# Performance work log

Hardware: AMD Instinct MI355X
Metric: run time of the kernel (lower is better)

The kernel has to match this reference:

```python
import jax, jax.numpy as jnp
import numpy as np
import math

B, R, D = 1, 2, 256
NH, NL, NP, ZA = 8, 1, 8, 4
H = W = 128
Q = H * W
HD = D // NH


def _bilinear(v, loc, Hl, Wl):
    # v: [BH, Hl*Wl, hd]; loc: [BH, Q, P, 2] normalized to [0,1]
    x = loc[..., 0] * Wl - 0.5
    y = loc[..., 1] * Hl - 0.5
    x0f = jnp.floor(x); y0f = jnp.floor(y)
    wx = (x - x0f)[..., None]; wy = (y - y0f)[..., None]
    x0 = x0f.astype(jnp.int32); y0 = y0f.astype(jnp.int32)
    def corner(iy, ix):
        valid = (iy >= 0) & (iy < Hl) & (ix >= 0) & (ix < Wl)
        idx = jnp.clip(iy, 0, Hl - 1) * Wl + jnp.clip(ix, 0, Wl - 1)
        g = jax.vmap(lambda vb, ib: vb[ib])(v, idx)  # [BH,Q,P,hd]
        return g * valid[..., None].astype(v.dtype)
    g00 = corner(y0, x0); g01 = corner(y0, x0 + 1)
    g10 = corner(y0 + 1, x0); g11 = corner(y0 + 1, x0 + 1)
    return (g00 * (1 - wx) + g01 * wx) * (1 - wy) + (g10 * (1 - wx) + g11 * wx) * wy


def setup_inputs() -> dict:
    key = jax.random.key(0)
    ks = jax.random.split(key, 12)
    query = jax.random.normal(ks[0], (B, Q, D), jnp.float32)
    value = jax.random.normal(ks[1], (B * R, Q, D), jnp.float32)
    reference_points = jax.random.uniform(ks[2], (R, Q, ZA, 2), jnp.float32)
    spatial_shapes = jnp.array([[H, W]], jnp.int32)
    # sampling_offsets: zero-ish weight + directional grid bias (as in init_weights)
    W_off = 0.01 * jax.random.normal(ks[3], (NH * NL * NP * 2, D), jnp.float32)
    thetas = jnp.arange(NH, dtype=jnp.float32) * (2.0 * math.pi / NH)
    grid = jnp.stack([jnp.cos(thetas), jnp.sin(thetas)], -1)
    grid = grid / jnp.max(jnp.abs(grid), axis=-1, keepdims=True)
    grid = jnp.tile(grid[:, None, None, :], (1, NL, NP, 1))
    grid = grid * (jnp.arange(1, NP + 1, dtype=jnp.float32)[None, None, :, None])
    b_off = grid.reshape(-1)
    W_attn = 0.01 * jax.random.normal(ks[4], (NH * NL * NP, D), jnp.float32)
    b_attn = 0.01 * jax.random.normal(ks[5], (NH * NL * NP,), jnp.float32)
    s = 1.0 / np.sqrt(D)
    W_val = s * jax.random.normal(ks[6], (D, D), jnp.float32)
    b_val = jnp.zeros((D,), jnp.float32)
    W_out = s * jax.random.normal(ks[7], (D, D), jnp.float32)
    b_out = jnp.zeros((D,), jnp.float32)
    return {"query": query, "value": value, "reference_points": reference_points,
            "spatial_shapes": spatial_shapes, "W_off": W_off, "b_off": b_off,
            "W_attn": W_attn, "b_attn": b_attn, "W_val": W_val, "b_val": b_val,
            "W_out": W_out, "b_out": b_out}


def reference(query, value, reference_points, spatial_shapes,
              W_off, b_off, W_attn, b_attn, W_val, b_val, W_out, b_out):
    shapes = np.asarray(spatial_shapes)  # static level shapes
    residual = query
    Bq, nq, d = query.shape
    Rr, _, za, _ = reference_points.shape
    # rebatch query/reference_points over histories -> batch Bq*Rr (== value batch)
    q = jnp.broadcast_to(query[:, None], (Bq, Rr, nq, d)).reshape(Bq * Rr, nq, d)
    rp = jnp.broadcast_to(reference_points[None], (Bq, Rr, nq, za, 2)).reshape(Bq * Rr, nq, za, 2)
    bs = value.shape[0]
    v = (value @ W_val.T + b_val).reshape(bs, -1, NH, HD)
    off = (q @ W_off.T + b_off).reshape(bs, nq, NH, NL, NP, 2)
    aw = jax.nn.softmax((q @ W_attn.T + b_attn).reshape(bs, nq, NH, NL * NP), axis=-1)
    aw = aw.reshape(bs, nq, NH, NL, NP)
    norm = jnp.stack([shapes[:, 1].astype(np.float32), shapes[:, 0].astype(np.float32)], -1)  # [NL,2] = (W,H)
    off = off / norm[None, None, None, :, None, :]
    off = off.reshape(bs, nq, NH, NL, NP // za, za, 2)
    loc = rp[:, :, None, None, None, :, :] + off  # [bs,nq,NH,NL,NP//za,za,2]
    loc = loc.reshape(bs, nq, NH, NL, NP, 2)
    # multi-scale deformable attention (gather + bilinear + weighted sum)
    starts = np.concatenate([[0], np.cumsum(shapes[:, 0] * shapes[:, 1])])
    out = jnp.zeros((bs * NH, nq, HD), v.dtype)
    for l in range(NL):
        Hl, Wl = int(shapes[l, 0]), int(shapes[l, 1])
        vl = v[:, starts[l]:starts[l + 1]].transpose(0, 2, 1, 3).reshape(bs * NH, Hl * Wl, HD)
        locl = loc[:, :, :, l].transpose(0, 2, 1, 3, 4).reshape(bs * NH, nq, NP, 2)
        sampled = _bilinear(vl, locl, Hl, Wl)  # [bs*NH, nq, NP, hd]
        awl = aw[:, :, :, l].transpose(0, 2, 1, 3).reshape(bs * NH, nq, NP)
        out = out + jnp.einsum('bqph,bqp->bqh', sampled, awl)
    out = out.reshape(bs, NH, nq, HD).transpose(0, 2, 1, 3).reshape(bs, nq, d)
    out = out.mean(0, keepdims=True)  # mean over history-batch dim -> [1,nq,d]
    out = out @ W_out.T + b_out
    return out + residual  # dropout is identity in eval
```

## Files before the change

kernel.cpp:

```cpp
#include <hip/hip_runtime.h>
#include <hip/hip_bf16.h>
#include <hip/hip_fp16.h>

#define QN 16384
#define DK 256

typedef float f4_t __attribute__((ext_vector_type(4)));
typedef short s16x8 __attribute__((ext_vector_type(8)));
typedef short s16x4 __attribute__((ext_vector_type(4)));
typedef unsigned int u32;
typedef u32 u32x4 __attribute__((ext_vector_type(4)));
typedef __fp16 h2_t __attribute__((ext_vector_type(2)));

__device__ inline short f2bf(float f){
  __hip_bfloat16 h = __float2bfloat16(f);
  return __builtin_bit_cast(short, h);
}
__device__ inline short f2h16(float f){
  __half h = __float2half(f);
  return __builtin_bit_cast(short, h);
}
__device__ inline float dot2h(u32 a, u32 b, float c){
#if __has_builtin(__builtin_amdgcn_fdot2)
  return __builtin_amdgcn_fdot2(__builtin_bit_cast(h2_t, a),
                                __builtin_bit_cast(h2_t, b), c, false);
#else
  h2_t ha = __builtin_bit_cast(h2_t, a), hb = __builtin_bit_cast(h2_t, b);
  return c + (float)ha[0] * (float)hb[0] + (float)ha[1] * (float)hb[1];
#endif
}
__device__ inline u32 pk2h(float a, float b){
#if __has_builtin(__builtin_amdgcn_cvt_pkrtz)
  h2_t r = __builtin_amdgcn_cvt_pkrtz(a, b);
  return __builtin_bit_cast(u32, r);
#else
  return (u32)__builtin_bit_cast(unsigned short, __float2half(a)) |
         ((u32)__builtin_bit_cast(unsigned short, __float2half(b)) << 16);
#endif
}
__device__ inline u32 bperm(u32 s0, u32 s1, u32 sel){
  return __builtin_amdgcn_perm(s0, s1, sel);
}

__global__ __launch_bounds__(256) void k_convw(const float* __restrict__ Wv,
    const float* __restrict__ Woff, const float* __restrict__ Wattn,
    const float* __restrict__ Wout, short* __restrict__ Wbf){
  const int row = blockIdx.x;
  const int c = threadIdx.x;
  const float* src;
  if (row < 256)       src = Wv    + (size_t)row * DK;
  else if (row < 384)  src = Woff  + (size_t)(row - 256) * DK;
  else if (row < 448)  src = Wattn + (size_t)(row - 384) * DK;
  else                 src = Wout  + (size_t)(row - 448) * DK;
  Wbf[(size_t)row * DK + c] = f2bf(src[c]);
}

__global__ __launch_bounds__(256, 2) void k_gemm_val(const float* __restrict__ A,
    const short* __restrict__ Bw, const float* __restrict__ bval,
    short* __restrict__ vhf){
  __shared__ short As[64 * 256];
  __shared__ short Bs[64 * 256];
  const int tid = threadIdx.x;
  const int lane = tid & 63, wv = tid >> 6;
  const int r16 = lane & 15, kh = lane >> 4;
  const int swsel = (r16 & 7) << 4;
  const int mbase = blockIdx.x * 64;

  #pragma unroll
  for (int i = 0; i < 16; ++i){
    const int lin = i * 256 + tid;
    const int r = lin >> 6, ck = lin & 63;
    const f4_t v = *(const f4_t*)(A + (size_t)(mbase + r) * DK + ck * 4);
    s16x4 o = { f2bf(v[0]), f2bf(v[1]), f2bf(v[2]), f2bf(v[3]) };
    *(s16x4*)((char*)As + r * 512 + ((ck * 8) ^ ((r & 7) << 4))) = o;
  }
  s16x8 breg[8];
  #pragma unroll
  for (int i = 0; i < 8; ++i){
    const int lin = i * 256 + tid;
    const int n = lin >> 5, ck = lin & 31;
    breg[i] = *(const s16x8*)(Bw + (size_t)n * DK + ck * 8);
  }
  __syncthreads();

  for (int cg = 0; cg < 4; ++cg){
    #pragma unroll
    for (int i = 0; i < 8; ++i){
      const int lin = i * 256 + tid;
      const int n = lin >> 5, ck = lin & 31;
      *(s16x8*)((char*)Bs + n * 512 + ((ck * 16) ^ ((n & 7) << 4))) = breg[i];
    }
    __syncthreads();
    if (cg < 3){
      #pragma unroll
      for (int i = 0; i < 8; ++i){
        const int lin = i * 256 + tid;
        const int n = lin >> 5, ck = lin & 31;
        breg[i] = *(const s16x8*)(Bw + (size_t)((cg + 1) * 64 + n) * DK + ck * 8);
      }
    }
    f4_t acc[4];
    #pragma unroll
    for (int i = 0; i < 4; ++i) acc[i] = (f4_t){0.f, 0.f, 0.f, 0.f};
    #pragma unroll
    for (int kk = 0; kk < 8; ++kk){
      const int kb = kh * 16 + kk * 64;
      const s16x8 a = *(const s16x8*)((char*)As + (wv * 16 + r16) * 512 + (kb ^ swsel));
      #pragma unroll
      for (int nt = 0; nt < 4; ++nt){
        const s16x8 b = *(const s16x8*)((char*)Bs + (nt * 16 + r16) * 512 + (kb ^ swsel));
        acc[nt] = __builtin_amdgcn_mfma_f32_16x16x32_bf16(a, b, acc[nt], 0, 0, 0);
      }
    }
    #pragma unroll
    for (int nt = 0; nt < 4; ++nt){
      const int n = cg * 64 + nt * 16 + r16;
      const int h = n >> 5, hd = n & 31;
      const float bv = bval[n];
      #pragma unroll
      for (int rix = 0; rix < 4; ++rix){
        const int m = mbase + wv * 16 + kh * 4 + rix;
        const int r = m >> 14, pix = m & (QN - 1);
        vhf[(size_t)((r * 8 + h) * QN + pix) * 32 + hd] = f2h16(acc[nt][rix] + bv);
      }
    }
    __syncthreads();
  }
}

__global__ __launch_bounds__(256, 2) void k_gemm_oa(const float* __restrict__ A,
    const short* __restrict__ Bw, const float* __restrict__ boff,
    const float* __restrict__ battn, float* __restrict__ offw,
    float* __restrict__ logit){
  __shared__ short As[32 * 256];
  __shared__ short Bs[64 * 256];
  const int tid = threadIdx.x;
  const int lane = tid & 63, wv = tid >> 6;
  const int r16 = lane & 15, kh = lane >> 4;
  const int mg = wv & 1, ch = wv >> 1;
  const int swsel = (r16 & 7) << 4;
  const int mbase = blockIdx.x * 32;

  #pragma unroll
  for (int i = 0; i < 8; ++i){
    const int lin = i * 256 + tid;
    const int r = lin >> 6, ck = lin & 63;
    const f4_t v = *(const f4_t*)(A + (size_t)(mbase + r) * DK + ck * 4);
    s16x4 o = { f2bf(v[0]), f2bf(v[1]), f2bf(v[2]), f2bf(v[3]) };
    *(s16x4*)((char*)As + r * 512 + ((ck * 8) ^ ((r & 7) << 4))) = o;
  }
  s16x8 breg[8];
  #pragma unroll
  for (int i = 0; i < 8; ++i){
    const int lin = i * 256 + tid;
    const int n = lin >> 5, ck = lin & 31;
    breg[i] = *(const s16x8*)(Bw + (size_t)n * DK + ck * 8);
  }
  __syncthreads();

  for (int cg = 0; cg < 3; ++cg){
    #pragma unroll
    for (int i = 0; i < 8; ++i){
      const int lin = i * 256 + tid;
      const int n = lin >> 5, ck = lin & 31;
      *(s16x8*)((char*)Bs + n * 512 + ((ck * 16) ^ ((n & 7) << 4))) = breg[i];
    }
    __syncthreads();
    if (cg < 2){
      #pragma unroll
      for (int i = 0; i < 8; ++i){
        const int lin = i * 256 + tid;
        const int n = lin >> 5, ck = lin & 31;
        breg[i] = *(const s16x8*)(Bw + (size_t)((cg + 1) * 64 + n) * DK + ck * 8);
      }
    }
    f4_t acc[2];
    acc[0] = (f4_t){0.f,0.f,0.f,0.f}; acc[1] = (f4_t){0.f,0.f,0.f,0.f};
    #pragma unroll
    for (int kk = 0; kk < 8; ++kk){
      const int kb = kh * 16 + kk * 64;
      const s16x8 a = *(const s16x8*)((char*)As + (mg * 16 + r16) * 512 + (kb ^ swsel));
      #pragma unroll
      for (int nt = 0; nt < 2; ++nt){
        const s16x8 b = *(const s16x8*)((char*)Bs + (ch * 32 + nt * 16 + r16) * 512 + (kb ^ swsel));
        acc[nt] = __builtin_amdgcn_mfma_f32_16x16x32_bf16(a, b, acc[nt], 0, 0, 0);
      }
    }
    #pragma unroll
    for (int nt = 0; nt < 2; ++nt){
      const int n = cg * 64 + ch * 32 + nt * 16 + r16;
      #pragma unroll
      for (int rix = 0; rix < 4; ++rix){
        const int m = mbase + mg * 16 + kh * 4 + rix;
        const float v = acc[nt][rix];
        if (n < 128) offw[(size_t)m * 128 + n] = v + boff[n];
        else         logit[(size_t)m * 64 + (n - 128)] = v + battn[n - 128];
      }
    }
    __syncthreads();
  }
}

__global__ __launch_bounds__(256, 2) void k_gemm_out(const short* __restrict__ Ab,
    const short* __restrict__ Bw, const float* __restrict__ bout,
    const float* __restrict__ query, float* __restrict__ out){
  __shared__ short As[32 * 256];
  __shared__ short Bs[64 * 256];
  const int tid = threadIdx.x;
  const int lane = tid & 63, wv = tid >> 6;
  const int r16 = lane & 15, kh = lane >> 4;
  const int mg = wv & 1, ch = wv >> 1;
  const int swsel = (r16 & 7) << 4;
  const int mbase = blockIdx.x * 32;

  #pragma unroll
  for (int i = 0; i < 4; ++i){
    const int lin = i * 256 + tid;
    const int r = lin >> 5, ck = lin & 31;
    const s16x8 v = *(const s16x8*)(Ab + (size_t)(mbase + r) * DK + ck * 8);
    *(s16x8*)((char*)As + r * 512 + ((ck * 16) ^ ((r & 7) << 4))) = v;
  }
  s16x8 breg[8];
  #pragma unroll
  for (int i = 0; i < 8; ++i){
    const int lin = i * 256 + tid;
    const int n = lin >> 5, ck = lin & 31;
    breg[i] = *(const s16x8*)(Bw + (size_t)n * DK + ck * 8);
  }
  __syncthreads();

  for (int cg = 0; cg < 4; ++cg){
    #pragma unroll
    for (int i = 0; i < 8; ++i){
      const int lin = i * 256 + tid;
      const int n = lin >> 5, ck = lin & 31;
      *(s16x8*)((char*)Bs + n * 512 + ((ck * 16) ^ ((n & 7) << 4))) = breg[i];
    }
    __syncthreads();
    if (cg < 3){
      #pragma unroll
      for (int i = 0; i < 8; ++i){
        const int lin = i * 256 + tid;
        const int n = lin >> 5, ck = lin & 31;
        breg[i] = *(const s16x8*)(Bw + (size_t)((cg + 1) * 64 + n) * DK + ck * 8);
      }
    }
    f4_t acc[2];
    acc[0] = (f4_t){0.f,0.f,0.f,0.f}; acc[1] = (f4_t){0.f,0.f,0.f,0.f};
    #pragma unroll
    for (int kk = 0; kk < 8; ++kk){
      const int kb = kh * 16 + kk * 64;
      const s16x8 a = *(const s16x8*)((char*)As + (mg * 16 + r16) * 512 + (kb ^ swsel));
      #pragma unroll
      for (int nt = 0; nt < 2; ++nt){
        const s16x8 b = *(const s16x8*)((char*)Bs + (ch * 32 + nt * 16 + r16) * 512 + (kb ^ swsel));
        acc[nt] = __builtin_amdgcn_mfma_f32_16x16x32_bf16(a, b, acc[nt], 0, 0, 0);
      }
    }
    #pragma unroll
    for (int nt = 0; nt < 2; ++nt){
      const int n = cg * 64 + ch * 32 + nt * 16 + r16;
      const float bo = bout[n];
      #pragma unroll
      for (int rix = 0; rix < 4; ++rix){
        const int m = mbase + mg * 16 + kh * 4 + rix;
        out[(size_t)m * DK + n] = acc[nt][rix] + bo + query[(size_t)m * DK + n];
      }
    }
    __syncthreads();
  }
}

__device__ inline void mkw(float rx, float ry, float ox, float oy, float awp,
                           u32& word, u32& pk01, u32& pk23){
  const float x = fmaf(rx, 128.f, ox) - 0.5f;
  const float y = fmaf(ry, 128.f, oy) - 0.5f;
  const float xf = floorf(x), yf = floorf(y);
  const float wx = x - xf, wy = y - yf;
  const int ix = (int)xf, iy = (int)yf;
  float xw0 = 1.f - wx, xw1 = wx, yw0 = 1.f - wy, yw1 = wy;
  if (ix < 0 || ix > 127)   xw0 = 0.f;
  if (ix < -1 || ix > 126)  xw1 = 0.f;
  if (iy < 0 || iy > 127)   yw0 = 0.f;
  if (iy < -1 || iy > 126)  yw1 = 0.f;
  const int ix0 = min(max(ix, 0), 127), ix1 = min(max(ix + 1, 0), 127);
  const int iy0 = min(max(iy, 0), 127), iy1 = min(max(iy + 1, 0), 127);
  const float t0 = awp * yw0, t1 = awp * yw1;
  pk01 = pk2h(t0 * xw0, t0 * xw1);
  pk23 = pk2h(t1 * xw0, t1 * xw1);
  word = (u32)(iy0 * 128 + ix0) | ((u32)(ix1 - ix0) << 16) | ((u32)(iy1 - iy0) << 17);
}

__global__ __launch_bounds__(256) void k_sampler(const float* __restrict__ rp,
    const float* __restrict__ offw, const float* __restrict__ logit,
    const short* __restrict__ vhf, short* __restrict__ O2b){
  const int tid = threadIdx.x;
  const int j3 = tid & 7;
  const int cj = j3 & 3;
  const int px = j3 >> 2;
  const int grp = tid >> 3;
  const int lane = tid & 63;
  const int glane8 = lane & ~7;
  const int h = blockIdx.x & 7;
  const int q = (blockIdx.x >> 3) * 32 + grp;
  const u32 cjof = (u32)cj * 8;
  const u32 selw = px ? 0x03020706u : 0x01000504u;

  const float* lp = logit + (size_t)q * 64 + h * 8;
  const float l = lp[j3];
  float m = l;
  m = fmaxf(m, __shfl_xor(m, 1)); m = fmaxf(m, __shfl_xor(m, 2)); m = fmaxf(m, __shfl_xor(m, 4));
  const float e = __expf(l - m);
  float ssum = e;
  ssum += __shfl_xor(ssum, 1); ssum += __shfl_xor(ssum, 2); ssum += __shfl_xor(ssum, 4);
  const float awp = e * (0.5f / ssum);

  const float* offp = offw + (size_t)q * 128 + h * 16;
  const float ox = offp[2 * j3], oy = offp[2 * j3 + 1];
  const int za2 = (j3 & 3) * 2;
  const float rx0 = rp[(size_t)q * 8 + za2],        ry0 = rp[(size_t)q * 8 + za2 + 1];
  const float rx1 = rp[(size_t)(QN + q) * 8 + za2], ry1 = rp[(size_t)(QN + q) * 8 + za2 + 1];

  u32 wrdA, pkA01, pkA23, wrdB, pkB01, pkB23;
  mkw(rx0, ry0, ox, oy, awp, wrdA, pkA01, pkA23);
  mkw(rx1, ry1, ox, oy, awp, wrdB, pkB01, pkB23);

  const short* vb0 = vhf + (size_t)(h * QN) * 32;
  const short* vb1 = vhf + (size_t)((8 + h) * QN) * 32;

  float acc[8] = {0.f,0.f,0.f,0.f,0.f,0.f,0.f,0.f};

#define STEP(S, WRD, PK01, PK23, VB) do{                                    \
    const int srcl_ = glane8 | ((S) & 7);                                   \
    const u32 wd_  = __shfl((WRD),  srcl_);                                 \
    const u32 w01_ = __shfl((PK01), srcl_);                                 \
    const u32 w23_ = __shfl((PK23), srcl_);                                 \
    const u32 wp_  = bperm(w01_, w23_, selw);     \
    const u32 o0_  = (wd_ & 0xFFFFu) * 32u + cjof                           \
                   + (px ? ((wd_ >> 11) & 32u) : 0u);                       \
    const u32 o1_  = o0_ + ((wd_ >> 17) & 1u) * 4096u;                      \
    const u32x4 cA_ = *(const u32x4*)((VB) + o0_);              \
    const u32x4 cB_ = *(const u32x4*)((VB) + o1_);              \
    _Pragma("unroll")                                                       \
    for (int e_ = 0; e_ < 4; ++e_){                                         \
      const u32 pl_ = bperm(cA_[e_], cB_[e_], 0x01000504u);                 \
      const u32 ph_ = bperm(cA_[e_], cB_[e_], 0x03020706u);                 \
      acc[2*e_]   = dot2h(pl_, wp_, acc[2*e_]);                             \
      acc[2*e_+1] = dot2h(ph_, wp_, acc[2*e_+1]);                           \
    }                                                                       \
  }while(0)

  STEP(0,  wrdA, pkA01, pkA23, vb0); STEP(1,  wrdA, pkA01, pkA23, vb0);
  STEP(2,  wrdA, pkA01, pkA23, vb0); STEP(3,  wrdA, pkA01, pkA23, vb0);
  STEP(4,  wrdA, pkA01, pkA23, vb0); STEP(5,  wrdA, pkA01, pkA23, vb0);
  STEP(6,  wrdA, pkA01, pkA23, vb0); STEP(7,  wrdA, pkA01, pkA23, vb0);
  STEP(8,  wrdB, pkB01, pkB23, vb1); STEP(9,  wrdB, pkB01, pkB23, vb1);
  STEP(10, wrdB, pkB01, pkB23, vb1); STEP(11, wrdB, pkB01, pkB23, vb1);
  STEP(12, wrdB, pkB01, pkB23, vb1); STEP(13, wrdB, pkB01, pkB23, vb1);
  STEP(14, wrdB, pkB01, pkB23, vb1); STEP(15, wrdB, pkB01, pkB23, vb1);
#undef STEP

  #pragma unroll
  for (int i = 0; i < 8; ++i) acc[i] += __shfl_xor(acc[i], 4);
  if (px == 0){
    s16x8 o = { f2bf(acc[0]), f2bf(acc[1]), f2bf(acc[2]), f2bf(acc[3]),
                f2bf(acc[4]), f2bf(acc[5]), f2bf(acc[6]), f2bf(acc[7]) };
    *(s16x8*)(O2b + (size_t)q * DK + h * 32 + cj * 8) = o;
  }
}

extern "C" void kernel_launch(void* const* d_in, const int* in_sizes, int n_in,
                              void* d_out, int out_size, void* d_ws, size_t ws_size,
                              hipStream_t stream) {
  const float* query = (const float*)d_in[0];
  const float* value = (const float*)d_in[1];
  const float* refpt = (const float*)d_in[2];
  const float* W_off  = (const float*)d_in[4];
  const float* b_off  = (const float*)d_in[5];
  const float* W_attn = (const float*)d_in[6];
  const float* b_attn = (const float*)d_in[7];
  const float* W_val  = (const float*)d_in[8];
  const float* b_val  = (const float*)d_in[9];
  const float* W_out  = (const float*)d_in[10];
  const float* b_out  = (const float*)d_in[11];
  float* out = (float*)d_out;

  char* ws = (char*)d_ws;
  short* Wbf  = (short*)(ws);
  short* vhf  = (short*)(ws + 360448);
  float* offw = (float*)(ws + 17137664);
  float* logit= (float*)(ws + 25526272);
  short* O2b  = (short*)(ws + 29720576);

  k_convw   <<<dim3(704),  dim3(256), 0, stream>>>(W_val, W_off, W_attn, W_out, Wbf);
  k_gemm_val<<<dim3(512),  dim3(256), 0, stream>>>(value, Wbf, b_val, vhf);
  k_gemm_oa <<<dim3(512),  dim3(256), 0, stream>>>(query, Wbf + 256 * DK, b_off, b_attn, offw, logit);
  k_sampler <<<dim3(4096), dim3(256), 0, stream>>>(refpt, offw, logit, vhf, O2b);
  k_gemm_out<<<dim3(512),  dim3(256), 0, stream>>>(O2b, Wbf + 448 * DK, b_out, query, out);
}
```

Measured before the change: 75.63 us.

## Merge value and offset/attention projections into one launch, pipeline sampler gathers

Combines the value projection GEMM and the offset/attention-logit GEMM into a single kernel that branches on block index, removing one launch and letting both projections run concurrently across the GPU. The weight-conversion kernel now processes 16 elements per thread with vectorized loads, using far fewer blocks. In the sampler, the gather loads for each sampling step are issued a few steps ahead of their use (software pipelining) to hide memory latency. The pipelining raises register pressure, and the merged kernel mixes two block shapes whose shared-memory and register footprints may differ.

```diff
diff --git a/kernel.cpp b/kernel.cpp
--- a/kernel.cpp
+++ b/kernel.cpp
@@ -45,159 +45,161 @@
 __global__ __launch_bounds__(256) void k_convw(const float* __restrict__ Wv,
     const float* __restrict__ Woff, const float* __restrict__ Wattn,
     const float* __restrict__ Wout, short* __restrict__ Wbf){
-  const int row = blockIdx.x;
-  const int c = threadIdx.x;
-  const float* src;
-  if (row < 256)       src = Wv    + (size_t)row * DK;
-  else if (row < 384)  src = Woff  + (size_t)(row - 256) * DK;
-  else if (row < 448)  src = Wattn + (size_t)(row - 384) * DK;
-  else                 src = Wout  + (size_t)(row - 448) * DK;
-  Wbf[(size_t)row * DK + c] = f2bf(src[c]);
-}
-
-__global__ __launch_bounds__(256, 2) void k_gemm_val(const float* __restrict__ A,
-    const short* __restrict__ Bw, const float* __restrict__ bval,
-    short* __restrict__ vhf){
+  const int base = (blockIdx.x * 256 + threadIdx.x) * 16;
+  #pragma unroll
+  for (int c = 0; c < 4; ++c){
+    const int e = base + c * 4;
+    const int row = e >> 8, col = e & 255;
+    const float* src;
+    int r = row;
+    if (row < 256)       src = Wv    + (size_t)r * DK;
+    else if (row < 384){ src = Woff  + (size_t)(r - 256) * DK; }
+    else if (row < 448){ src = Wattn + (size_t)(r - 384) * DK; }
+    else               { src = Wout  + (size_t)(r - 448) * DK; }
+    const f4_t v = *(const f4_t*)(src + col);
+    s16x4 o = { f2bf(v[0]), f2bf(v[1]), f2bf(v[2]), f2bf(v[3]) };
+    *(s16x4*)(Wbf + e) = o;
+  }
+}
+
+__global__ __launch_bounds__(256, 2) void k_proj(const float* __restrict__ value,
+    const float* __restrict__ query, const short* __restrict__ Wbf,
+    const float* __restrict__ bval, const float* __restrict__ boff,
+    const float* __restrict__ battn, short* __restrict__ vhf,
+    float* __restrict__ offw, float* __restrict__ logit){
   __shared__ short As[64 * 256];
   __shared__ short Bs[64 * 256];
   const int tid = threadIdx.x;
   const int lane = tid & 63, wv = tid >> 6;
   const int r16 = lane & 15, kh = lane >> 4;
   const int swsel = (r16 & 7) << 4;
-  const int mbase = blockIdx.x * 64;
-
-  #pragma unroll
-  for (int i = 0; i < 16; ++i){
-    const int lin = i * 256 + tid;
-    const int r = lin >> 6, ck = lin & 63;
-    const f4_t v = *(const f4_t*)(A + (size_t)(mbase + r) * DK + ck * 4);
-    s16x4 o = { f2bf(v[0]), f2bf(v[1]), f2bf(v[2]), f2bf(v[3]) };
-    *(s16x4*)((char*)As + r * 512 + ((ck * 8) ^ ((r & 7) << 4))) = o;
-  }
-  s16x8 breg[8];
-  #pragma unroll
-  for (int i = 0; i < 8; ++i){
-    const int lin = i * 256 + tid;
-    const int n = lin >> 5, ck = lin & 31;
-    breg[i] = *(const s16x8*)(Bw + (size_t)n * DK + ck * 8);
-  }
-  __syncthreads();
-
-  for (int cg = 0; cg < 4; ++cg){
+  const int bid = blockIdx.x;
+
+  if (bid < 512){
+    const float* A = value;
+    const short* Bw = Wbf;
+    const int mbase = bid * 64;
+    #pragma unroll
+    for (int i = 0; i < 16; ++i){
+      const int lin = i * 256 + tid;
+      const int r = lin >> 6, ck = lin & 63;
+      const f4_t v = *(const f4_t*)(A + (size_t)(mbase + r) * DK + ck * 4);
+      s16x4 o = { f2bf(v[0]), f2bf(v[1]), f2bf(v[2]), f2bf(v[3]) };
+      *(s16x4*)((char*)As + r * 512 + ((ck * 8) ^ ((r & 7) << 4))) = o;
+    }
+    s16x8 breg[8];
     #pragma unroll
     for (int i = 0; i < 8; ++i){
       const int lin = i * 256 + tid;
       const int n = lin >> 5, ck = lin & 31;
-      *(s16x8*)((char*)Bs + n * 512 + ((ck * 16) ^ ((n & 7) << 4))) = breg[i];
+      breg[i] = *(const s16x8*)(Bw + (size_t)n * DK + ck * 8);
     }
     __syncthreads();
-    if (cg < 3){
+    for (int cg = 0; cg < 4; ++cg){
       #pragma unroll
       for (int i = 0; i < 8; ++i){
         const int lin = i * 256 + tid;
         const int n = lin >> 5, ck = lin & 31;
-        breg[i] = *(const s16x8*)(Bw + (size_t)((cg + 1) * 64 + n) * DK + ck * 8);
-      }
-    }
-    f4_t acc[4];
-    #pragma unroll
-    for (int i = 0; i < 4; ++i) acc[i] = (f4_t){0.f, 0.f, 0.f, 0.f};
-    #pragma unroll
-    for (int kk = 0; kk < 8; ++kk){
-      const int kb = kh * 16 + kk * 64;
-      const s16x8 a = *(const s16x8*)((char*)As + (wv * 16 + r16) * 512 + (kb ^ swsel));
+        *(s16x8*)((char*)Bs + n * 512 + ((ck * 16) ^ ((n & 7) << 4))) = breg[i];
+      }
+      __syncthreads();
+      if (cg < 3){
+        #pragma unroll
+        for (int i = 0; i < 8; ++i){
+          const int lin = i * 256 + tid;
+          const int n = lin >> 5, ck = lin & 31;
+          breg[i] = *(const s16x8*)(Bw + (size_t)((cg + 1) * 64 + n) * DK + ck * 8);
+        }
+      }
+      f4_t acc[4];
+      #pragma unroll
+      for (int i = 0; i < 4; ++i) acc[i] = (f4_t){0.f, 0.f, 0.f, 0.f};
+      #pragma unroll
+      for (int kk = 0; kk < 8; ++kk){
+        const int kb = kh * 16 + kk * 64;
+        const s16x8 a = *(const s16x8*)((char*)As + (wv * 16 + r16) * 512 + (kb ^ swsel));
+        #pragma unroll
+        for (int nt = 0; nt < 4; ++nt){
+          const s16x8 b = *(const s16x8*)((char*)Bs + (nt * 16 + r16) * 512 + (kb ^ swsel));
+          acc[nt] = __builtin_amdgcn_mfma_f32_16x16x32_bf16(a, b, acc[nt], 0, 0, 0);
+        }
+      }
       #pragma unroll
       for (int nt = 0; nt < 4; ++nt){
-        const s16x8 b = *(const s16x8*)((char*)Bs + (nt * 16 + r16) * 512 + (kb ^ swsel));
-        acc[nt] = __builtin_amdgcn_mfma_f32_16x16x32_bf16(a, b, acc[nt], 0, 0, 0);
-      }
-    }
-    #pragma unroll
-    for (int nt = 0; nt < 4; ++nt){
-      const int n = cg * 64 + nt * 16 + r16;
-      const int h = n >> 5, hd = n & 31;
-      const float bv = bval[n];
-      #pragma unroll
-      for (int rix = 0; rix < 4; ++rix){
-        const int m = mbase + wv * 16 + kh * 4 + rix;
-        const int r = m >> 14, pix = m & (QN - 1);
-        vhf[(size_t)((r * 8 + h) * QN + pix) * 32 + hd] = f2h16(acc[nt][rix] + bv);
-      }
-    }
-    __syncthreads();
-  }
-}
-
-__global__ __launch_bounds__(256, 2) void k_gemm_oa(const float* __restrict__ A,
-    const short* __restrict__ Bw, const float* __restrict__ boff,
-    const float* __restrict__ battn, float* __restrict__ offw,
-    float* __restrict__ logit){
-  __shared__ short As[32 * 256];
-  __shared__ short Bs[64 * 256];
-  const int tid = threadIdx.x;
-  const int lane = tid & 63, wv = tid >> 6;
-  const int r16 = lane & 15, kh = lane >> 4;
-  const int mg = wv & 1, ch = wv >> 1;
-  const int swsel = (r16 & 7) << 4;
-  const int mbase = blockIdx.x * 32;
-
-  #pragma unroll
-  for (int i = 0; i < 8; ++i){
-    const int lin = i * 256 + tid;
-    const int r = lin >> 6, ck = lin & 63;
-    const f4_t v = *(const f4_t*)(A + (size_t)(mbase + r) * DK + ck * 4);
-    s16x4 o = { f2bf(v[0]), f2bf(v[1]), f2bf(v[2]), f2bf(v[3]) };
-    *(s16x4*)((char*)As + r * 512 + ((ck * 8) ^ ((r & 7) << 4))) = o;
-  }
-  s16x8 breg[8];
-  #pragma unroll
-  for (int i = 0; i < 8; ++i){
-    const int lin = i * 256 + tid;
-    const int n = lin >> 5, ck = lin & 31;
-    breg[i] = *(const s16x8*)(Bw + (size_t)n * DK + ck * 8);
-  }
-  __syncthreads();
-
-  for (int cg = 0; cg < 3; ++cg){
+        const int n = cg * 64 + nt * 16 + r16;
+        const int h = n >> 5, hd = n & 31;
+        const float bv = bval[n];
+        #pragma unroll
+        for (int rix = 0; rix < 4; ++rix){
+          const int m = mbase + wv * 16 + kh * 4 + rix;
+          const int r = m >> 14, pix = m & (QN - 1);
+          vhf[(size_t)((r * 8 + h) * QN + pix) * 32 + hd] = f2h16(acc[nt][rix] + bv);
+        }
+      }
+      __syncthreads();
+    }
+  } else {
+    const float* A = query;
+    const short* Bw = Wbf + 256 * DK;
+    const int mg = wv & 1, ch = wv >> 1;
+    const int mbase = (bid - 512) * 32;
+    #pragma unroll
+    for (int i = 0; i < 8; ++i){
+      const int lin = i * 256 + tid;
+      const int r = lin >> 6, ck = lin & 63;
+      const f4_t v = *(const f4_t*)(A + (size_t)(mbase + r) * DK + ck * 4);
+      s16x4 o = { f2bf(v[0]), f2bf(v[1]), f2bf(v[2]), f2bf(v[3]) };
+      *(s16x4*)((char*)As + r * 512 + ((ck * 8) ^ ((r & 7) << 4))) = o;
+    }
+    s16x8 breg[8];
     #pragma unroll
     for (int i = 0; i < 8; ++i){
       const int lin = i * 256 + tid;
       const int n = lin >> 5, ck = lin & 31;
-      *(s16x8*)((char*)Bs + n * 512 + ((ck * 16) ^ ((n & 7) << 4))) = breg[i];
+      breg[i] = *(const s16x8*)(Bw + (size_t)n * DK + ck * 8);
     }
     __syncthreads();
-    if (cg < 2){
+    for (int cg = 0; cg < 3; ++cg){
       #pragma unroll
       for (int i = 0; i < 8; ++i){
         const int lin = i * 256 + tid;
         const int n = lin >> 5, ck = lin & 31;
-        breg[i] = *(const s16x8*)(Bw + (size_t)((cg + 1) * 64 + n) * DK + ck * 8);
-      }
-    }
-    f4_t acc[2];
-    acc[0] = (f4_t){0.f,0.f,0.f,0.f}; acc[1] = (f4_t){0.f,0.f,0.f,0.f};
-    #pragma unroll
-    for (int kk = 0; kk < 8; ++kk){
-      const int kb = kh * 16 + kk * 64;
-      const s16x8 a = *(const s16x8*)((char*)As + (mg * 16 + r16) * 512 + (kb ^ swsel));
+        *(s16x8*)((char*)Bs + n * 512 + ((ck * 16) ^ ((n & 7) << 4))) = breg[i];
+      }
+      __syncthreads();
+      if (cg < 2){
+        #pragma unroll
+        for (int i = 0; i < 8; ++i){
+          const int lin = i * 256 + tid;
+          const int n = lin >> 5, ck = lin & 31;
+          breg[i] = *(const s16x8*)(Bw + (size_t)((cg + 1) * 64 + n) * DK + ck * 8);
+        }
+      }
+      f4_t acc[2];
+      acc[0] = (f4_t){0.f,0.f,0.f,0.f}; acc[1] = (f4_t){0.f,0.f,0.f,0.f};
+      #pragma unroll
+      for (int kk = 0; kk < 8; ++kk){
+        const int kb = kh * 16 + kk * 64;
+        const s16x8 a = *(const s16x8*)((char*)As + (mg * 16 + r16) * 512 + (kb ^ swsel));
+        #pragma unroll
+        for (int nt = 0; nt < 2; ++nt){
+          const s16x8 b = *(const s16x8*)((char*)Bs + (ch * 32 + nt * 16 + r16) * 512 + (kb ^ swsel));
+          acc[nt] = __builtin_amdgcn_mfma_f32_16x16x32_bf16(a, b, acc[nt], 0, 0, 0);
+        }
+      }
       #pragma unroll
       for (int nt = 0; nt < 2; ++nt){
-        const s16x8 b = *(const s16x8*)((char*)Bs + (ch * 32 + nt * 16 + r16) * 512 + (kb ^ swsel));
-        acc[nt] = __builtin_amdgcn_mfma_f32_16x16x32_bf16(a, b, acc[nt], 0, 0, 0);
-      }
-    }
-    #pragma unroll
-    for (int nt = 0; nt < 2; ++nt){
-      const int n = cg * 64 + ch * 32 + nt * 16 + r16;
-      #pragma unroll
-      for (int rix = 0; rix < 4; ++rix){
-        const int m = mbase + mg * 16 + kh * 4 + rix;
-        const float v = acc[nt][rix];
-        if (n < 128) offw[(size_t)m * 128 + n] = v + boff[n];
-        else         logit[(size_t)m * 64 + (n - 128)] = v + battn[n - 128];
-      }
-    }
-    __syncthreads();
+        const int n = cg * 64 + ch * 32 + nt * 16 + r16;
+        #pragma unroll
+        for (int rix = 0; rix < 4; ++rix){
+          const int m = mbase + mg * 16 + kh * 4 + rix;
+          const float v = acc[nt][rix];
+          if (n < 128) offw[(size_t)m * 128 + n] = v + boff[n];
+          else         logit[(size_t)m * 64 + (n - 128)] = v + battn[n - 128];
+        }
+      }
+      __syncthreads();
+    }
   }
 }
 
@@ -330,35 +332,47 @@
 
   float acc[8] = {0.f,0.f,0.f,0.f,0.f,0.f,0.f,0.f};
 
-#define STEP(S, WRD, PK01, PK23, VB) do{                                    \
+#define LOADP(S, WRD, VB)                                                   \
+  const u32 wd_##S = __shfl((WRD), glane8 | ((S) & 7));                     \
+  const u32 o0_##S = (wd_##S & 0xFFFFu) * 32u + cjof                        \
+                   + (px ? ((wd_##S >> 11) & 32u) : 0u);                    \
+  const u32 o1_##S = o0_##S + ((wd_##S >> 17) & 1u) * 4096u;                \
+  const u32x4 cA_##S = *(const u32x4*)((VB) + o0_##S);                      \
+  const u32x4 cB_##S = *(const u32x4*)((VB) + o1_##S);
+
+#define USEP(S, PK01, PK23) do{                                             \
     const int srcl_ = glane8 | ((S) & 7);                                   \
-    const u32 wd_  = __shfl((WRD),  srcl_);                                 \
     const u32 w01_ = __shfl((PK01), srcl_);                                 \
     const u32 w23_ = __shfl((PK23), srcl_);                                 \
-    const u32 wp_  = bperm(w01_, w23_, selw);     \
-    const u32 o0_  = (wd_ & 0xFFFFu) * 32u + cjof                           \
-                   + (px ? ((wd_ >> 11) & 32u) : 0u);                       \
-    const u32 o1_  = o0_ + ((wd_ >> 17) & 1u) * 4096u;                      \
-    const u32x4 cA_ = *(const u32x4*)((VB) + o0_);              \
-    const u32x4 cB_ = *(const u32x4*)((VB) + o1_);              \
+    const u32 wp_  = bperm(w01_, w23_, selw);                               \
     _Pragma("unroll")                                                       \
     for (int e_ = 0; e_ < 4; ++e_){                                         \
-      const u32 pl_ = bperm(cA_[e_], cB_[e_], 0x01000504u);                 \
-      const u32 ph_ = bperm(cA_[e_], cB_[e_], 0x03020706u);                 \
+      const u32 pl_ = bperm(cA_##S[e_], cB_##S[e_], 0x01000504u);           \
+      const u32 ph_ = bperm(cA_##S[e_], cB_##S[e_], 0x03020706u);           \
       acc[2*e_]   = dot2h(pl_, wp_, acc[2*e_]);                             \
       acc[2*e_+1] = dot2h(ph_, wp_, acc[2*e_+1]);                           \
     }                                                                       \
   }while(0)
 
-  STEP(0,  wrdA, pkA01, pkA23, vb0); STEP(1,  wrdA, pkA01, pkA23, vb0);
-  STEP(2,  wrdA, pkA01, pkA23, vb0); STEP(3,  wrdA, pkA01, pkA23, vb0);
-  STEP(4,  wrdA, pkA01, pkA23, vb0); STEP(5,  wrdA, pkA01, pkA23, vb0);
-  STEP(6,  wrdA, pkA01, pkA23, vb0); STEP(7,  wrdA, pkA01, pkA23, vb0);
-  STEP(8,  wrdB, pkB01, pkB23, vb1); STEP(9,  wrdB, pkB01, pkB23, vb1);
-  STEP(10, wrdB, pkB01, pkB23, vb1); STEP(11, wrdB, pkB01, pkB23, vb1);
-  STEP(12, wrdB, pkB01, pkB23, vb1); STEP(13, wrdB, pkB01, pkB23, vb1);
-  STEP(14, wrdB, pkB01, pkB23, vb1); STEP(15, wrdB, pkB01, pkB23, vb1);
-#undef STEP
+  LOADP(0,  wrdA, vb0) LOADP(1,  wrdA, vb0) LOADP(2,  wrdA, vb0)
+  USEP(0,  pkA01, pkA23); LOADP(3,  wrdA, vb0)
+  USEP(1,  pkA01, pkA23); LOADP(4,  wrdA, vb0)
+  USEP(2,  pkA01, pkA23); LOADP(5,  wrdA, vb0)
+  USEP(3,  pkA01, pkA23); LOADP(6,  wrdA, vb0)
+  USEP(4,  pkA01, pkA23); LOADP(7,  wrdA, vb0)
+  USEP(5,  pkA01, pkA23); LOADP(8,  wrdB, vb1)
+  USEP(6,  pkA01, pkA23); LOADP(9,  wrdB, vb1)
+  USEP(7,  pkA01, pkA23); LOADP(10, wrdB, vb1)
+  USEP(8,  pkB01, pkB23); LOADP(11, wrdB, vb1)
+  USEP(9,  pkB01, pkB23); LOADP(12, wrdB, vb1)
+  USEP(10, pkB01, pkB23); LOADP(13, wrdB, vb1)
+  USEP(11, pkB01, pkB23); LOADP(14, wrdB, vb1)
+  USEP(12, pkB01, pkB23); LOADP(15, wrdB, vb1)
+  USEP(13, pkB01, pkB23);
+  USEP(14, pkB01, pkB23);
+  USEP(15, pkB01, pkB23);
+#undef LOADP
+#undef USEP
 
   #pragma unroll
   for (int i = 0; i < 8; ++i) acc[i] += __shfl_xor(acc[i], 4);
@@ -392,9 +406,9 @@
   float* logit= (float*)(ws + 25526272);
   short* O2b  = (short*)(ws + 29720576);
 
-  k_convw   <<<dim3(704),  dim3(256), 0, stream>>>(W_val, W_off, W_attn, W_out, Wbf);
-  k_gemm_val<<<dim3(512),  dim3(256), 0, stream>>>(value, Wbf, b_val, vhf);
-  k_gemm_oa <<<dim3(512),  dim3(256), 0, stream>>>(query, Wbf + 256 * DK, b_off, b_attn, offw, logit);
+  k_convw   <<<dim3(44),   dim3(256), 0, stream>>>(W_val, W_off, W_attn, W_out, Wbf);
+  k_proj    <<<dim3(1024), dim3(256), 0, stream>>>(value, query, Wbf, b_val, b_off,
+                                                   b_attn, vhf, offw, logit);
   k_sampler <<<dim3(4096), dim3(256), 0, stream>>>(refpt, offw, logit, vhf, O2b);
   k_gemm_out<<<dim3(512),  dim3(256), 0, stream>>>(O2b, Wbf + 448 * DK, b_out, query, out);
 }
```

Result: faster. 71.88 us (-5.0%).
